# Kernel optimization log

Measured on AMD Instinct MI355X. Metric: run time of the kernel, lower is better.

The kernel has to match this reference:

```python
import jax, jax.numpy as jnp
import numpy as np

DIM_Q = 512
DIM_K = 512
DIM_V = 512
NUM_HEADS = 8
LN_EPS = 1e-5


def setup_inputs() -> dict:
    key = jax.random.key(0)
    ks = jax.random.split(key, 12)
    s_q = 1.0 / np.sqrt(DIM_Q)
    s_k = 1.0 / np.sqrt(DIM_K)
    s_v = 1.0 / np.sqrt(DIM_V)
    return {
        "Q": jax.random.normal(ks[0], (8, 1024, DIM_Q), dtype=jnp.float32),
        "K": jax.random.normal(ks[1], (8, 1024, DIM_K), dtype=jnp.float32),
        "Wq": jax.random.uniform(ks[2], (DIM_Q, DIM_V), jnp.float32, -s_q, s_q),
        "bq": jax.random.uniform(ks[3], (DIM_V,), jnp.float32, -s_q, s_q),
        "Wk": jax.random.uniform(ks[4], (DIM_K, DIM_V), jnp.float32, -s_k, s_k),
        "bk": jax.random.uniform(ks[5], (DIM_V,), jnp.float32, -s_k, s_k),
        "Wv": jax.random.uniform(ks[6], (DIM_K, DIM_V), jnp.float32, -s_k, s_k),
        "bv": jax.random.uniform(ks[7], (DIM_V,), jnp.float32, -s_k, s_k),
        "Wo": jax.random.uniform(ks[8], (DIM_V, DIM_V), jnp.float32, -s_v, s_v),
        "bo": jax.random.uniform(ks[9], (DIM_V,), jnp.float32, -s_v, s_v),
        "g0": jnp.ones((DIM_V,), jnp.float32),
        "b0": jnp.zeros((DIM_V,), jnp.float32),
        "g1": jnp.ones((DIM_V,), jnp.float32),
        "b1": jnp.zeros((DIM_V,), jnp.float32),
    }


def _layer_norm(x, gamma, beta):
    mu = jnp.mean(x, axis=-1, keepdims=True)
    var = jnp.var(x, axis=-1, keepdims=True)
    return (x - mu) * jax.lax.rsqrt(var + LN_EPS) * gamma + beta


def reference(Q, K, Wq, bq, Wk, bk, Wv, bv, Wo, bo, g0, b0, g1, b1):
    B, Nq, _ = Q.shape
    Nk = K.shape[1]
    H = NUM_HEADS
    d = DIM_V // H  # head dim

    Qp = Q @ Wq + bq                      # [B, Nq, dim_V]
    Kp = K @ Wk + bk                      # [B, Nk, dim_V]
    Vp = K @ Wv + bv                      # [B, Nk, dim_V]

    Qh = Qp.reshape(B, Nq, H, d)
    Kh = Kp.reshape(B, Nk, H, d)
    Vh = Vp.reshape(B, Nk, H, d)

    scores = jnp.einsum("bqhd,bkhd->bhqk", Qh, Kh) / jnp.sqrt(jnp.float32(d))
    A = jax.nn.softmax(scores, axis=-1)   # [B, H, Nq, Nk]
    Oh = jnp.einsum("bhqk,bkhd->bqhd", A, Vh) + Qh  # residual with projected Q
    O = Oh.reshape(B, Nq, DIM_V)

    O = _layer_norm(O, g0, b0)
    O = O + jax.nn.relu(O @ Wo + bo)
    O = _layer_norm(O, g1, b1)
    return O
```

## Files before the change

kernel.cpp:

```cpp
#include <hip/hip_runtime.h>
#include <math.h>

#define DV 512
#define HD 64
#define NHEADS 8
#define SEQ 1024
#define NBATCH 8
#define MROWS (NBATCH * SEQ)

typedef __bf16 bf16;
typedef __bf16 bf16x8 __attribute__((ext_vector_type(8)));
typedef __bf16 bf16x4 __attribute__((ext_vector_type(4)));
typedef float f32x4 __attribute__((ext_vector_type(4)));

__device__ inline void gload_lds16(const void* g, void* l) {
  __builtin_amdgcn_global_load_lds(
      (const __attribute__((address_space(1))) unsigned int*)g,
      (__attribute__((address_space(3))) unsigned int*)l, 16, 0, 0);
}

__global__ __launch_bounds__(256) void prep_kernel(
    const float* __restrict__ Qf, const float* __restrict__ Kf,
    bf16* __restrict__ Qb, bf16* __restrict__ Kb,
    const float* __restrict__ W0, const float* __restrict__ W1,
    const float* __restrict__ W2, const float* __restrict__ W3,
    bf16* __restrict__ T0, bf16* __restrict__ T1,
    bf16* __restrict__ T2, bf16* __restrict__ T3)
{
  const int z = blockIdx.z;
  if (z < 2) {
    const float* src = z ? Kf : Qf;
    bf16* dst = z ? Kb : Qb;
    int i = blockIdx.x * 256 + threadIdx.x;
    const float4* s = (const float4*)src;
    float4 a = s[i * 2], b = s[i * 2 + 1];
    bf16x8 o;
    o[0] = (bf16)a.x; o[1] = (bf16)a.y; o[2] = (bf16)a.z; o[3] = (bf16)a.w;
    o[4] = (bf16)b.x; o[5] = (bf16)b.y; o[6] = (bf16)b.z; o[7] = (bf16)b.w;
    *(bf16x8*)(dst + (size_t)i * 8) = o;
    return;
  }
  if (blockIdx.x >= 64) return;
  const float* W = z == 2 ? W0 : z == 3 ? W1 : z == 4 ? W2 : W3;
  bf16* WT = z == 2 ? T0 : z == 3 ? T1 : z == 4 ? T2 : T3;
  __shared__ float T[64][65];
  const int t = threadIdx.x;
  const int k0 = (blockIdx.x >> 3) * 64, n0 = (blockIdx.x & 7) * 64;
#pragma unroll
  for (int p = 0; p < 4; ++p) {
    int r = p * 16 + (t >> 4), c = (t & 15) * 4;
    float4 v = *(const float4*)&W[(size_t)(k0 + r) * DV + n0 + c];
    T[r][c] = v.x; T[r][c + 1] = v.y; T[r][c + 2] = v.z; T[r][c + 3] = v.w;
  }
  __syncthreads();
#pragma unroll
  for (int p = 0; p < 2; ++p) {
    int n = p * 32 + (t >> 3), kc = (t & 7) * 8;
    bf16x8 o;
#pragma unroll
    for (int j = 0; j < 8; ++j) o[j] = (bf16)T[kc + j][n];
    *(bf16x8*)&WT[(size_t)(n0 + n) * DV + k0 + kc] = o;
  }
}

__device__ __forceinline__ void gemm_core128_db(
    const bf16* __restrict__ A, const bf16* __restrict__ B,
    bf16* As, bf16* Bs, int m0, int n0, int Kd, f32x4 (*acc)[4])
{
  const int tid = threadIdx.x;
  const int lane = tid & 63, w = tid >> 6;
  const int wm = w >> 1, wn = w & 1;
  const int cl = lane & 15, qd = lane >> 4;

  size_t offA[4], offB[4];
  int ldsOff[4];
#pragma unroll
  for (int t = 0; t < 4; ++t) {
    int S = t * 256 + tid;
    int row = S >> 3, kq = (S & 7) ^ (row & 7);
    offA[t] = (size_t)(m0 + row) * Kd + kq * 8;
    offB[t] = (size_t)(n0 + row) * Kd + kq * 8;
    ldsOff[t] = (t * 256 + w * 64) * 8;
  }

#pragma unroll
  for (int t = 0; t < 4; ++t) {
    gload_lds16(A + offA[t], As + ldsOff[t]);
    gload_lds16(B + offB[t], Bs + ldsOff[t]);
  }

  const int nIter = Kd >> 6;
  for (int it = 0; it < nIter; ++it) {
    __syncthreads();
    const int cur = it & 1;
    if (it + 1 < nIter) {
      const size_t k0n = (size_t)(it + 1) * 64;
      const int nb = (cur ^ 1) * 8192;
#pragma unroll
      for (int t = 0; t < 4; ++t) {
        gload_lds16(A + k0n + offA[t], As + nb + ldsOff[t]);
        gload_lds16(B + k0n + offB[t], Bs + nb + ldsOff[t]);
      }
    }
    const bf16* A_ = As + cur * 8192;
    const bf16* B_ = Bs + cur * 8192;
#pragma unroll
    for (int cc = 0; cc < 2; ++cc) {
      bf16x8 af[4], bfr[4];
#pragma unroll
      for (int mi = 0; mi < 4; ++mi) {
        int row = wm * 64 + mi * 16 + cl;
        int slot = row * 8 + ((cc * 4 + qd) ^ (row & 7));
        af[mi] = *(const bf16x8*)(A_ + (size_t)slot * 8);
      }
#pragma unroll
      for (int ni = 0; ni < 4; ++ni) {
        int row = wn * 64 + ni * 16 + cl;
        int slot = row * 8 + ((cc * 4 + qd) ^ (row & 7));
        bfr[ni] = *(const bf16x8*)(B_ + (size_t)slot * 8);
      }
#pragma unroll
      for (int mi = 0; mi < 4; ++mi)
#pragma unroll
        for (int ni = 0; ni < 4; ++ni)
          acc[mi][ni] = __builtin_amdgcn_mfma_f32_16x16x32_bf16(
              af[mi], bfr[ni], acc[mi][ni], 0, 0, 0);
    }
  }
}

__global__ __launch_bounds__(256) void gemm_proj(
    const bf16* __restrict__ A0, const bf16* __restrict__ A1, const bf16* __restrict__ A2,
    const bf16* __restrict__ B0, const bf16* __restrict__ B1, const bf16* __restrict__ B2,
    const float* __restrict__ c0, const float* __restrict__ c1, const float* __restrict__ c2,
    bf16* __restrict__ O0, bf16* __restrict__ O1, bf16* __restrict__ O2)
{
  __shared__ bf16 As[2 * 128 * 64];
  __shared__ bf16 Bs[2 * 128 * 64];
  const int z = blockIdx.z;
  const bf16* A = z == 0 ? A0 : z == 1 ? A1 : A2;
  const bf16* B = z == 0 ? B0 : z == 1 ? B1 : B2;
  const float* bias = z == 0 ? c0 : z == 1 ? c1 : c2;
  bf16* C = z == 0 ? O0 : z == 1 ? O1 : O2;
  const int N = (z == 2) ? MROWS : DV;
  int bx, by;
  if (z < 2) { bx = blockIdx.x & 3;  by = blockIdx.x >> 2; }
  else       { bx = blockIdx.x & 63; by = blockIdx.x >> 6; }
  const int m0 = by * 128, n0 = bx * 128;

  f32x4 acc[4][4] = {};
  gemm_core128_db(A, B, As, Bs, m0, n0, DV, acc);

  const int lane = threadIdx.x & 63, w = threadIdx.x >> 6;
  const int wm = w >> 1, wn = w & 1;
  const int cl = lane & 15, qd = lane >> 4;
  float bcol[4] = {0.f, 0.f, 0.f, 0.f};
  if (z < 2)
#pragma unroll
    for (int ni = 0; ni < 4; ++ni) bcol[ni] = bias[n0 + wn * 64 + ni * 16 + cl];
#pragma unroll
  for (int mi = 0; mi < 4; ++mi)
#pragma unroll
    for (int r = 0; r < 4; ++r) {
      int gm = m0 + wm * 64 + mi * 16 + qd * 4 + r;
      float brow = (z == 2) ? bias[gm] : 0.f;
#pragma unroll
      for (int ni = 0; ni < 4; ++ni) {
        int gn = n0 + wn * 64 + ni * 16 + cl;
        float v = acc[mi][ni][r] + (z == 2 ? brow : bcol[ni]);
        C[(size_t)gm * N + gn] = (bf16)v;
      }
    }
}

__global__ __launch_bounds__(256) void gemm_out(
    const bf16* __restrict__ A, const bf16* __restrict__ B,
    const float* __restrict__ bias, const bf16* __restrict__ res,
    float* __restrict__ Cout)
{
  __shared__ bf16 As[2 * 128 * 64];
  __shared__ bf16 Bs[2 * 64 * 64];
  const int tid = threadIdx.x;
  const int lane = tid & 63, w = tid >> 6;
  const int wm = w >> 1, wn = w & 1;
  const int cl = lane & 15, qd = lane >> 4;
  const int m0 = blockIdx.y * 128, n0 = blockIdx.x * 64;

  size_t offA[4], offB[2];
  int ldsA[4], ldsB[2];
#pragma unroll
  for (int t = 0; t < 4; ++t) {
    int S = t * 256 + tid;
    int row = S >> 3, kq = (S & 7) ^ (row & 7);
    offA[t] = (size_t)(m0 + row) * DV + kq * 8;
    ldsA[t] = (t * 256 + w * 64) * 8;
  }
#pragma unroll
  for (int t = 0; t < 2; ++t) {
    int S = t * 256 + tid;
    int row = S >> 3, kq = (S & 7) ^ (row & 7);
    offB[t] = (size_t)(n0 + row) * DV + kq * 8;
    ldsB[t] = (t * 256 + w * 64) * 8;
  }

#pragma unroll
  for (int t = 0; t < 4; ++t) gload_lds16(A + offA[t], As + ldsA[t]);
#pragma unroll
  for (int t = 0; t < 2; ++t) gload_lds16(B + offB[t], Bs + ldsB[t]);

  f32x4 acc[4][2] = {};
  for (int it = 0; it < DV / 64; ++it) {
    __syncthreads();
    const int cur = it & 1;
    if (it + 1 < DV / 64) {
      const size_t k0n = (size_t)(it + 1) * 64;
#pragma unroll
      for (int t = 0; t < 4; ++t)
        gload_lds16(A + k0n + offA[t], As + (cur ^ 1) * 8192 + ldsA[t]);
#pragma unroll
      for (int t = 0; t < 2; ++t)
        gload_lds16(B + k0n + offB[t], Bs + (cur ^ 1) * 4096 + ldsB[t]);
    }
    const bf16* A_ = As + cur * 8192;
    const bf16* B_ = Bs + cur * 4096;
#pragma unroll
    for (int cc = 0; cc < 2; ++cc) {
      bf16x8 af[4], bfr[2];
#pragma unroll
      for (int mi = 0; mi < 4; ++mi) {
        int row = wm * 64 + mi * 16 + cl;
        int slot = row * 8 + ((cc * 4 + qd) ^ (row & 7));
        af[mi] = *(const bf16x8*)(A_ + (size_t)slot * 8);
      }
#pragma unroll
      for (int ni = 0; ni < 2; ++ni) {
        int row = wn * 32 + ni * 16 + cl;
        int slot = row * 8 + ((cc * 4 + qd) ^ (row & 7));
        bfr[ni] = *(const bf16x8*)(B_ + (size_t)slot * 8);
      }
#pragma unroll
      for (int mi = 0; mi < 4; ++mi)
#pragma unroll
        for (int ni = 0; ni < 2; ++ni)
          acc[mi][ni] = __builtin_amdgcn_mfma_f32_16x16x32_bf16(
              af[mi], bfr[ni], acc[mi][ni], 0, 0, 0);
    }
  }

  float bcol[2] = { bias[n0 + wn * 32 + cl], bias[n0 + wn * 32 + 16 + cl] };
#pragma unroll
  for (int mi = 0; mi < 4; ++mi)
#pragma unroll
    for (int r = 0; r < 4; ++r) {
      int gm = m0 + wm * 64 + mi * 16 + qd * 4 + r;
#pragma unroll
      for (int ni = 0; ni < 2; ++ni) {
        int gn = n0 + wn * 32 + ni * 16 + cl;
        size_t off = (size_t)gm * DV + gn;
        float v = acc[mi][ni][r] + bcol[ni];
        Cout[off] = (float)res[off] + fmaxf(v, 0.f);
      }
    }
}

__global__ __launch_bounds__(256) void attn_mfma(
    const bf16* __restrict__ Qp, const bf16* __restrict__ Kp,
    const bf16* __restrict__ VpT, bf16* __restrict__ Orb)
{
  __shared__ bf16 Ks[2][64 * 64];
  __shared__ bf16 Vs[2][64 * 64];
  __shared__ bf16 Ps[4][32 * 72];

  const int tid = threadIdx.x, lane = tid & 63, w = tid >> 6;
  const int cl = lane & 15, qd = lane >> 4;
  const int bh = blockIdx.y, b = bh >> 3, h = bh & 7;
  const int q0w = blockIdx.x * 128 + w * 32;

  const float SCL = 0.18033688011112042f;
  bf16x8 qa[2][2];
#pragma unroll
  for (int qt = 0; qt < 2; ++qt)
#pragma unroll
    for (int ch = 0; ch < 2; ++ch) {
      bf16x8 v = *(const bf16x8*)(Qp + ((size_t)b * SEQ + q0w + qt * 16 + cl) * DV
                                  + h * HD + ch * 32 + qd * 8);
#pragma unroll
      for (int j = 0; j < 8; ++j) v[j] = (bf16)((float)v[j] * SCL);
      qa[qt][ch] = v;
    }

  f32x4 o[4][2] = {};
  float lrun[2] = {0.f, 0.f};

  const bf16* Kbase = Kp + (size_t)b * SEQ * DV + h * HD;
  const bf16* Vbase = VpT + (size_t)h * HD * MROWS + (size_t)b * SEQ;
  bf16* Pw = &Ps[w][0];

  const int Sa = tid, Sb = 256 + tid;
  const int kRowA = Sa >> 3, kDgA = (Sa & 7) ^ (kRowA & 7);
  const int kRowB = Sb >> 3, kDgB = (Sb & 7) ^ (kRowB & 7);
  const size_t kOffA = (size_t)kRowA * DV + kDgA * 8;
  const size_t kOffB = (size_t)kRowB * DV + kDgB * 8;
  const size_t vOffA = (size_t)kRowA * MROWS + kDgA * 8;
  const size_t vOffB = (size_t)kRowB * MROWS + kDgB * 8;

  gload_lds16(Kbase + kOffA, &Ks[0][(size_t)(w * 64) * 8]);
  gload_lds16(Kbase + kOffB, &Ks[0][(size_t)(256 + w * 64) * 8]);
  gload_lds16(Vbase + vOffA, &Vs[0][(size_t)(w * 64) * 8]);
  gload_lds16(Vbase + vOffB, &Vs[0][(size_t)(256 + w * 64) * 8]);

  for (int it = 0; it < SEQ / 64; ++it) {
    __syncthreads();
    const int cur = it & 1;
    if (it + 1 < SEQ / 64) {
      const size_t kt = (size_t)(it + 1) * 64;
      gload_lds16(Kbase + kt * DV + kOffA, &Ks[cur ^ 1][(size_t)(w * 64) * 8]);
      gload_lds16(Kbase + kt * DV + kOffB, &Ks[cur ^ 1][(size_t)(256 + w * 64) * 8]);
      gload_lds16(Vbase + kt + vOffA, &Vs[cur ^ 1][(size_t)(w * 64) * 8]);
      gload_lds16(Vbase + kt + vOffB, &Vs[cur ^ 1][(size_t)(256 + w * 64) * 8]);
    }
    const bf16* K_ = &Ks[cur][0];
    const bf16* V_ = &Vs[cur][0];

    f32x4 sc[4][2] = {};
#pragma unroll
    for (int ch = 0; ch < 2; ++ch) {
      bf16x8 kf[4];
#pragma unroll
      for (int kt4 = 0; kt4 < 4; ++kt4) {
        int key = kt4 * 16 + cl;
        int slot = key * 8 + ((ch * 4 + qd) ^ (key & 7));
        kf[kt4] = *(const bf16x8*)(K_ + (size_t)slot * 8);
      }
#pragma unroll
      for (int kt4 = 0; kt4 < 4; ++kt4)
#pragma unroll
        for (int qt = 0; qt < 2; ++qt)
          sc[kt4][qt] = __builtin_amdgcn_mfma_f32_16x16x32_bf16(
              kf[kt4], qa[qt][ch], sc[kt4][qt], 0, 0, 0);
    }

#pragma unroll
    for (int qt = 0; qt < 2; ++qt) {
      float sum = 0.f;
#pragma unroll
      for (int kt4 = 0; kt4 < 4; ++kt4) {
        float p0 = __builtin_amdgcn_exp2f(sc[kt4][qt][0]);
        float p1 = __builtin_amdgcn_exp2f(sc[kt4][qt][1]);
        float p2 = __builtin_amdgcn_exp2f(sc[kt4][qt][2]);
        float p3 = __builtin_amdgcn_exp2f(sc[kt4][qt][3]);
        sum += (p0 + p1) + (p2 + p3);
        bf16x4 pk;
        pk[0] = (bf16)p0; pk[1] = (bf16)p1; pk[2] = (bf16)p2; pk[3] = (bf16)p3;
        *(bf16x4*)(Pw + (size_t)(qt * 16 + cl) * 72 + kt4 * 16 + qd * 4) = pk;
      }
      sum += __shfl_xor(sum, 16);
      sum += __shfl_xor(sum, 32);
      lrun[qt] += sum;
    }

#pragma unroll
    for (int kc = 0; kc < 2; ++kc) {
      bf16x8 pb[2];
#pragma unroll
      for (int qt = 0; qt < 2; ++qt)
        pb[qt] = *(const bf16x8*)(Pw + (size_t)(qt * 16 + cl) * 72 + kc * 32 + qd * 8);
#pragma unroll
      for (int dt = 0; dt < 4; ++dt) {
        int d = dt * 16 + cl;
        int slot = d * 8 + ((kc * 4 + qd) ^ (d & 7));
        bf16x8 vf = *(const bf16x8*)(V_ + (size_t)slot * 8);
#pragma unroll
        for (int qt = 0; qt < 2; ++qt)
          o[dt][qt] = __builtin_amdgcn_mfma_f32_16x16x32_bf16(
              vf, pb[qt], o[dt][qt], 0, 0, 0);
      }
    }
  }

#pragma unroll
  for (int qt = 0; qt < 2; ++qt) {
    float inv = 1.f / lrun[qt];
    size_t rowoff = ((size_t)b * SEQ + q0w + qt * 16 + cl) * DV + h * HD;
#pragma unroll
    for (int dt = 0; dt < 4; ++dt) {
      bf16x4 rv = *(const bf16x4*)(Qp + rowoff + dt * 16 + qd * 4);
      bf16x4 st;
      st[0] = (bf16)(o[dt][qt][0] * inv + (float)rv[0]);
      st[1] = (bf16)(o[dt][qt][1] * inv + (float)rv[1]);
      st[2] = (bf16)(o[dt][qt][2] * inv + (float)rv[2]);
      st[3] = (bf16)(o[dt][qt][3] * inv + (float)rv[3]);
      *(bf16x4*)(Orb + rowoff + dt * 16 + qd * 4) = st;
    }
  }
}

__global__ __launch_bounds__(256) void ln_bf16(
    const bf16* __restrict__ X, const float* __restrict__ g,
    const float* __restrict__ be, bf16* __restrict__ Y)
{
  const int row = blockIdx.x * 4 + (threadIdx.x >> 6);
  const int l = threadIdx.x & 63;
  bf16x8 xv = *(const bf16x8*)(X + (size_t)row * DV + l * 8);
  float x[8];
#pragma unroll
  for (int j = 0; j < 8; ++j) x[j] = (float)xv[j];
  float s = 0.f, s2 = 0.f;
#pragma unroll
  for (int j = 0; j < 8; ++j) { s += x[j]; s2 += x[j] * x[j]; }
#pragma unroll
  for (int off = 1; off < 64; off <<= 1) {
    s += __shfl_xor(s, off);
    s2 += __shfl_xor(s2, off);
  }
  float mu = s * (1.f / DV);
  float var = s2 * (1.f / DV) - mu * mu;
  float inv = rsqrtf(var + 1e-5f);
  float4 g1 = ((const float4*)(g + l * 8))[0], g2 = ((const float4*)(g + l * 8))[1];
  float4 b1 = ((const float4*)(be + l * 8))[0], b2 = ((const float4*)(be + l * 8))[1];
  bf16x8 ov;
  ov[0] = (bf16)((x[0] - mu) * inv * g1.x + b1.x);
  ov[1] = (bf16)((x[1] - mu) * inv * g1.y + b1.y);
  ov[2] = (bf16)((x[2] - mu) * inv * g1.z + b1.z);
  ov[3] = (bf16)((x[3] - mu) * inv * g1.w + b1.w);
  ov[4] = (bf16)((x[4] - mu) * inv * g2.x + b2.x);
  ov[5] = (bf16)((x[5] - mu) * inv * g2.y + b2.y);
  ov[6] = (bf16)((x[6] - mu) * inv * g2.z + b2.z);
  ov[7] = (bf16)((x[7] - mu) * inv * g2.w + b2.w);
  *(bf16x8*)(Y + (size_t)row * DV + l * 8) = ov;
}

__global__ __launch_bounds__(256) void ln_inplace(
    float* __restrict__ X, const float* __restrict__ g, const float* __restrict__ be)
{
  const int row = blockIdx.x * 4 + (threadIdx.x >> 6);
  const int l = threadIdx.x & 63;
  float* x = X + (size_t)row * DV + l * 8;
  float4 a = ((const float4*)x)[0], c = ((const float4*)x)[1];
  float s  = (a.x + a.y) + (a.z + a.w) + (c.x + c.y) + (c.z + c.w);
  float s2 = a.x*a.x + a.y*a.y + a.z*a.z + a.w*a.w + c.x*c.x + c.y*c.y + c.z*c.z + c.w*c.w;
#pragma unroll
  for (int off = 1; off < 64; off <<= 1) {
    s += __shfl_xor(s, off);
    s2 += __shfl_xor(s2, off);
  }
  float mu = s * (1.f / DV);
  float var = s2 * (1.f / DV) - mu * mu;
  float inv = rsqrtf(var + 1e-5f);
  float4 g1 = ((const float4*)(g + l * 8))[0], g2 = ((const float4*)(g + l * 8))[1];
  float4 b1 = ((const float4*)(be + l * 8))[0], b2 = ((const float4*)(be + l * 8))[1];
  a.x = (a.x - mu) * inv * g1.x + b1.x;
  a.y = (a.y - mu) * inv * g1.y + b1.y;
  a.z = (a.z - mu) * inv * g1.z + b1.z;
  a.w = (a.w - mu) * inv * g1.w + b1.w;
  c.x = (c.x - mu) * inv * g2.x + b2.x;
  c.y = (c.y - mu) * inv * g2.y + b2.y;
  c.z = (c.z - mu) * inv * g2.z + b2.z;
  c.w = (c.w - mu) * inv * g2.w + b2.w;
  ((float4*)x)[0] = a;
  ((float4*)x)[1] = c;
}

extern "C" void kernel_launch(void* const* d_in, const int* in_sizes, int n_in,
                              void* d_out, int out_size, void* d_ws, size_t ws_size,
                              hipStream_t stream)
{
  const float* Q  = (const float*)d_in[0];
  const float* Kf = (const float*)d_in[1];
  const float* Wq = (const float*)d_in[2];
  const float* bq = (const float*)d_in[3];
  const float* Wk = (const float*)d_in[4];
  const float* bk = (const float*)d_in[5];
  const float* Wv = (const float*)d_in[6];
  const float* bv = (const float*)d_in[7];
  const float* Wo = (const float*)d_in[8];
  const float* bo = (const float*)d_in[9];
  const float* g0 = (const float*)d_in[10];
  const float* b0 = (const float*)d_in[11];
  const float* g1 = (const float*)d_in[12];
  const float* b1 = (const float*)d_in[13];
  float* out = (float*)d_out;

  const size_t MB = 1ull << 20;
  char* W = (char*)d_ws;
  bf16* Qb  = (bf16*)(W + 0);
  bf16* Kb  = (bf16*)(W + 8 * MB);
  bf16* Qp  = (bf16*)(W + 16 * MB);
  bf16* Kp  = (bf16*)(W + 24 * MB);
  bf16* VpT = (bf16*)(W + 32 * MB);
  bf16* WqT = (bf16*)(W + 40 * MB);
  bf16* WkT = (bf16*)(W + 40 * MB + 512 * 1024);
  bf16* WvT = (bf16*)(W + 41 * MB);
  bf16* WoT = (bf16*)(W + 41 * MB + 512 * 1024);
  bf16* Xb  = (bf16*)(W + 42 * MB);
  bf16* Orb = (bf16*)(W + 0);

  dim3 blk(256);
  prep_kernel<<<dim3(2048, 1, 6), blk, 0, stream>>>(
      Q, Kf, Qb, Kb, Wq, Wk, Wv, Wo, WqT, WkT, WvT, WoT);
  gemm_proj<<<dim3(256, 1, 3), blk, 0, stream>>>(
      Qb, Kb, WvT, WqT, WkT, Kb, bq, bk, bv, Qp, Kp, VpT);
  attn_mfma<<<dim3(SEQ / 128, NBATCH * NHEADS), blk, 0, stream>>>(Qp, Kp, VpT, Orb);
  ln_bf16<<<dim3(MROWS / 4), blk, 0, stream>>>(Orb, g0, b0, Xb);
  gemm_out<<<dim3(DV / 64, MROWS / 128), blk, 0, stream>>>(Xb, WoT, bo, Xb, out);
  ln_inplace<<<dim3(MROWS / 4), blk, 0, stream>>>(out, g1, b1);
}
```

Measured before the change: 190.8 us.

## Fuse fp32-to-bf16 cast into projection GEMM and fuse LN0+out-GEMM+LN1

The projection GEMM now reads the fp32 Q and K directly, converting to bf16 in registers before storing to LDS. This removes the separate cast pass and its bf16 round-trip through memory. The tail is merged into one kernel: it layer-normalises a 32-row tile into LDS, multiplies it by WoT streamed in 32-wide k-chunks, then applies bias, ReLU and residual and runs the second layer norm in registers with a cross-wave reduction. This cuts three launches and several full-tensor round-trips, at the cost of heavy register use (64 floats plus a y array), fewer blocks, and a single-buffered WoT load with two barriers per iteration.

```diff
diff --git a/kernel.cpp b/kernel.cpp
--- a/kernel.cpp
+++ b/kernel.cpp
@@ -19,30 +19,15 @@
       (__attribute__((address_space(3))) unsigned int*)l, 16, 0, 0);
 }
 
-__global__ __launch_bounds__(256) void prep_kernel(
-    const float* __restrict__ Qf, const float* __restrict__ Kf,
-    bf16* __restrict__ Qb, bf16* __restrict__ Kb,
+__global__ __launch_bounds__(256) void prep_w(
     const float* __restrict__ W0, const float* __restrict__ W1,
     const float* __restrict__ W2, const float* __restrict__ W3,
     bf16* __restrict__ T0, bf16* __restrict__ T1,
     bf16* __restrict__ T2, bf16* __restrict__ T3)
 {
   const int z = blockIdx.z;
-  if (z < 2) {
-    const float* src = z ? Kf : Qf;
-    bf16* dst = z ? Kb : Qb;
-    int i = blockIdx.x * 256 + threadIdx.x;
-    const float4* s = (const float4*)src;
-    float4 a = s[i * 2], b = s[i * 2 + 1];
-    bf16x8 o;
-    o[0] = (bf16)a.x; o[1] = (bf16)a.y; o[2] = (bf16)a.z; o[3] = (bf16)a.w;
-    o[4] = (bf16)b.x; o[5] = (bf16)b.y; o[6] = (bf16)b.z; o[7] = (bf16)b.w;
-    *(bf16x8*)(dst + (size_t)i * 8) = o;
-    return;
-  }
-  if (blockIdx.x >= 64) return;
-  const float* W = z == 2 ? W0 : z == 3 ? W1 : z == 4 ? W2 : W3;
-  bf16* WT = z == 2 ? T0 : z == 3 ? T1 : z == 4 ? T2 : T3;
+  const float* W = z == 0 ? W0 : z == 1 ? W1 : z == 2 ? W2 : W3;
+  bf16* WT = z == 0 ? T0 : z == 1 ? T1 : z == 2 ? T2 : T3;
   __shared__ float T[64][65];
   const int t = threadIdx.x;
   const int k0 = (blockIdx.x >> 3) * 64, n0 = (blockIdx.x & 7) * 64;
@@ -63,9 +48,10 @@
   }
 }
 
-__device__ __forceinline__ void gemm_core128_db(
-    const bf16* __restrict__ A, const bf16* __restrict__ B,
-    bf16* As, bf16* Bs, int m0, int n0, int Kd, f32x4 (*acc)[4])
+template<bool AF, bool BF>
+__device__ __forceinline__ void proj_core(
+    const float* Af, const bf16* Ab, const float* Bf, const bf16* Bb,
+    bf16* As, bf16* Bs, int m0, int n0, f32x4 (*acc)[4])
 {
   const int tid = threadIdx.x;
   const int lane = tid & 63, w = tid >> 6;
@@ -73,33 +59,58 @@
   const int cl = lane & 15, qd = lane >> 4;
 
   size_t offA[4], offB[4];
-  int ldsOff[4];
+  int uOff[4], sOff[4];
 #pragma unroll
   for (int t = 0; t < 4; ++t) {
     int S = t * 256 + tid;
     int row = S >> 3, kq = (S & 7) ^ (row & 7);
-    offA[t] = (size_t)(m0 + row) * Kd + kq * 8;
-    offB[t] = (size_t)(n0 + row) * Kd + kq * 8;
-    ldsOff[t] = (t * 256 + w * 64) * 8;
-  }
+    offA[t] = (size_t)(m0 + row) * DV + kq * 8;
+    offB[t] = (size_t)(n0 + row) * DV + kq * 8;
+    uOff[t] = (t * 256 + w * 64) * 8;
+    sOff[t] = S * 8;
+  }
+
+  float4 ra0[4], ra1[4], rb0[4], rb1[4];
 
 #pragma unroll
   for (int t = 0; t < 4; ++t) {
-    gload_lds16(A + offA[t], As + ldsOff[t]);
-    gload_lds16(B + offB[t], Bs + ldsOff[t]);
-  }
-
-  const int nIter = Kd >> 6;
-  for (int it = 0; it < nIter; ++it) {
+    if (AF) {
+      ra0[t] = *(const float4*)(Af + offA[t]);
+      ra1[t] = *(const float4*)(Af + offA[t] + 4);
+      bf16x8 o;
+      o[0]=(bf16)ra0[t].x; o[1]=(bf16)ra0[t].y; o[2]=(bf16)ra0[t].z; o[3]=(bf16)ra0[t].w;
+      o[4]=(bf16)ra1[t].x; o[5]=(bf16)ra1[t].y; o[6]=(bf16)ra1[t].z; o[7]=(bf16)ra1[t].w;
+      *(bf16x8*)(As + sOff[t]) = o;
+    } else {
+      gload_lds16(Ab + offA[t], As + uOff[t]);
+    }
+    if (BF) {
+      rb0[t] = *(const float4*)(Bf + offB[t]);
+      rb1[t] = *(const float4*)(Bf + offB[t] + 4);
+      bf16x8 o;
+      o[0]=(bf16)rb0[t].x; o[1]=(bf16)rb0[t].y; o[2]=(bf16)rb0[t].z; o[3]=(bf16)rb0[t].w;
+      o[4]=(bf16)rb1[t].x; o[5]=(bf16)rb1[t].y; o[6]=(bf16)rb1[t].z; o[7]=(bf16)rb1[t].w;
+      *(bf16x8*)(Bs + sOff[t]) = o;
+    } else {
+      gload_lds16(Bb + offB[t], Bs + uOff[t]);
+    }
+  }
+
+  for (int it = 0; it < 8; ++it) {
     __syncthreads();
     const int cur = it & 1;
-    if (it + 1 < nIter) {
-      const size_t k0n = (size_t)(it + 1) * 64;
-      const int nb = (cur ^ 1) * 8192;
+    const int nb = (cur ^ 1) * 8192;
+    const bool has = (it + 1 < 8);
+    const size_t k0n = (size_t)(it + 1) * 64;
+    if (has) {
 #pragma unroll
       for (int t = 0; t < 4; ++t) {
-        gload_lds16(A + k0n + offA[t], As + nb + ldsOff[t]);
-        gload_lds16(B + k0n + offB[t], Bs + nb + ldsOff[t]);
+        if (AF) { ra0[t] = *(const float4*)(Af + k0n + offA[t]);
+                  ra1[t] = *(const float4*)(Af + k0n + offA[t] + 4); }
+        else    gload_lds16(Ab + k0n + offA[t], As + nb + uOff[t]);
+        if (BF) { rb0[t] = *(const float4*)(Bf + k0n + offB[t]);
+                  rb1[t] = *(const float4*)(Bf + k0n + offB[t] + 4); }
+        else    gload_lds16(Bb + k0n + offB[t], Bs + nb + uOff[t]);
       }
     }
     const bf16* A_ = As + cur * 8192;
@@ -126,30 +137,48 @@
           acc[mi][ni] = __builtin_amdgcn_mfma_f32_16x16x32_bf16(
               af[mi], bfr[ni], acc[mi][ni], 0, 0, 0);
     }
+    if (has) {
+#pragma unroll
+      for (int t = 0; t < 4; ++t) {
+        if (AF) {
+          bf16x8 o;
+          o[0]=(bf16)ra0[t].x; o[1]=(bf16)ra0[t].y; o[2]=(bf16)ra0[t].z; o[3]=(bf16)ra0[t].w;
+          o[4]=(bf16)ra1[t].x; o[5]=(bf16)ra1[t].y; o[6]=(bf16)ra1[t].z; o[7]=(bf16)ra1[t].w;
+          *(bf16x8*)(As + nb + sOff[t]) = o;
+        }
+        if (BF) {
+          bf16x8 o;
+          o[0]=(bf16)rb0[t].x; o[1]=(bf16)rb0[t].y; o[2]=(bf16)rb0[t].z; o[3]=(bf16)rb0[t].w;
+          o[4]=(bf16)rb1[t].x; o[5]=(bf16)rb1[t].y; o[6]=(bf16)rb1[t].z; o[7]=(bf16)rb1[t].w;
+          *(bf16x8*)(Bs + nb + sOff[t]) = o;
+        }
+      }
+    }
   }
 }
 
 __global__ __launch_bounds__(256) void gemm_proj(
-    const bf16* __restrict__ A0, const bf16* __restrict__ A1, const bf16* __restrict__ A2,
-    const bf16* __restrict__ B0, const bf16* __restrict__ B1, const bf16* __restrict__ B2,
-    const float* __restrict__ c0, const float* __restrict__ c1, const float* __restrict__ c2,
-    bf16* __restrict__ O0, bf16* __restrict__ O1, bf16* __restrict__ O2)
+    const float* __restrict__ Qf, const float* __restrict__ Kf,
+    const bf16* __restrict__ WqT, const bf16* __restrict__ WkT,
+    const bf16* __restrict__ WvT,
+    const float* __restrict__ bq, const float* __restrict__ bk,
+    const float* __restrict__ bv,
+    bf16* __restrict__ Qp, bf16* __restrict__ Kp, bf16* __restrict__ VpT)
 {
-  __shared__ bf16 As[2 * 128 * 64];
-  __shared__ bf16 Bs[2 * 128 * 64];
+  __shared__ bf16 As[2 * 8192];
+  __shared__ bf16 Bs[2 * 8192];
   const int z = blockIdx.z;
-  const bf16* A = z == 0 ? A0 : z == 1 ? A1 : A2;
-  const bf16* B = z == 0 ? B0 : z == 1 ? B1 : B2;
-  const float* bias = z == 0 ? c0 : z == 1 ? c1 : c2;
-  bf16* C = z == 0 ? O0 : z == 1 ? O1 : O2;
-  const int N = (z == 2) ? MROWS : DV;
-  int bx, by;
-  if (z < 2) { bx = blockIdx.x & 3;  by = blockIdx.x >> 2; }
-  else       { bx = blockIdx.x & 63; by = blockIdx.x >> 6; }
+  int bx, by, N;
+  if (z < 2) { bx = blockIdx.x & 3;  by = blockIdx.x >> 2; N = DV; }
+  else       { bx = blockIdx.x & 63; by = blockIdx.x >> 6; N = MROWS; }
   const int m0 = by * 128, n0 = bx * 128;
 
   f32x4 acc[4][4] = {};
-  gemm_core128_db(A, B, As, Bs, m0, n0, DV, acc);
+  const float* bias;
+  bf16* C;
+  if (z == 0) { proj_core<true,  false>(Qf, nullptr, nullptr, WqT, As, Bs, m0, n0, acc); bias = bq; C = Qp; }
+  else if (z == 1) { proj_core<true,  false>(Kf, nullptr, nullptr, WkT, As, Bs, m0, n0, acc); bias = bk; C = Kp; }
+  else { proj_core<false, true>(nullptr, WvT, Kf, nullptr, As, Bs, m0, n0, acc); bias = bv; C = VpT; }
 
   const int lane = threadIdx.x & 63, w = threadIdx.x >> 6;
   const int wm = w >> 1, wn = w & 1;
@@ -169,96 +198,6 @@
         int gn = n0 + wn * 64 + ni * 16 + cl;
         float v = acc[mi][ni][r] + (z == 2 ? brow : bcol[ni]);
         C[(size_t)gm * N + gn] = (bf16)v;
-      }
-    }
-}
-
-__global__ __launch_bounds__(256) void gemm_out(
-    const bf16* __restrict__ A, const bf16* __restrict__ B,
-    const float* __restrict__ bias, const bf16* __restrict__ res,
-    float* __restrict__ Cout)
-{
-  __shared__ bf16 As[2 * 128 * 64];
-  __shared__ bf16 Bs[2 * 64 * 64];
-  const int tid = threadIdx.x;
-  const int lane = tid & 63, w = tid >> 6;
-  const int wm = w >> 1, wn = w & 1;
-  const int cl = lane & 15, qd = lane >> 4;
-  const int m0 = blockIdx.y * 128, n0 = blockIdx.x * 64;
-
-  size_t offA[4], offB[2];
-  int ldsA[4], ldsB[2];
-#pragma unroll
-  for (int t = 0; t < 4; ++t) {
-    int S = t * 256 + tid;
-    int row = S >> 3, kq = (S & 7) ^ (row & 7);
-    offA[t] = (size_t)(m0 + row) * DV + kq * 8;
-    ldsA[t] = (t * 256 + w * 64) * 8;
-  }
-#pragma unroll
-  for (int t = 0; t < 2; ++t) {
-    int S = t * 256 + tid;
-    int row = S >> 3, kq = (S & 7) ^ (row & 7);
-    offB[t] = (size_t)(n0 + row) * DV + kq * 8;
-    ldsB[t] = (t * 256 + w * 64) * 8;
-  }
-
-#pragma unroll
-  for (int t = 0; t < 4; ++t) gload_lds16(A + offA[t], As + ldsA[t]);
-#pragma unroll
-  for (int t = 0; t < 2; ++t) gload_lds16(B + offB[t], Bs + ldsB[t]);
-
-  f32x4 acc[4][2] = {};
-  for (int it = 0; it < DV / 64; ++it) {
-    __syncthreads();
-    const int cur = it & 1;
-    if (it + 1 < DV / 64) {
-      const size_t k0n = (size_t)(it + 1) * 64;
-#pragma unroll
-      for (int t = 0; t < 4; ++t)
-        gload_lds16(A + k0n + offA[t], As + (cur ^ 1) * 8192 + ldsA[t]);
-#pragma unroll
-      for (int t = 0; t < 2; ++t)
-        gload_lds16(B + k0n + offB[t], Bs + (cur ^ 1) * 4096 + ldsB[t]);
-    }
-    const bf16* A_ = As + cur * 8192;
-    const bf16* B_ = Bs + cur * 4096;
-#pragma unroll
-    for (int cc = 0; cc < 2; ++cc) {
-      bf16x8 af[4], bfr[2];
-#pragma unroll
-      for (int mi = 0; mi < 4; ++mi) {
-        int row = wm * 64 + mi * 16 + cl;
-        int slot = row * 8 + ((cc * 4 + qd) ^ (row & 7));
-        af[mi] = *(const bf16x8*)(A_ + (size_t)slot * 8);
-      }
-#pragma unroll
-      for (int ni = 0; ni < 2; ++ni) {
-        int row = wn * 32 + ni * 16 + cl;
-        int slot = row * 8 + ((cc * 4 + qd) ^ (row & 7));
-        bfr[ni] = *(const bf16x8*)(B_ + (size_t)slot * 8);
-      }
-#pragma unroll
-      for (int mi = 0; mi < 4; ++mi)
-#pragma unroll
-        for (int ni = 0; ni < 2; ++ni)
-          acc[mi][ni] = __builtin_amdgcn_mfma_f32_16x16x32_bf16(
-              af[mi], bfr[ni], acc[mi][ni], 0, 0, 0);
-    }
-  }
-
-  float bcol[2] = { bias[n0 + wn * 32 + cl], bias[n0 + wn * 32 + 16 + cl] };
-#pragma unroll
-  for (int mi = 0; mi < 4; ++mi)
-#pragma unroll
-    for (int r = 0; r < 4; ++r) {
-      int gm = m0 + wm * 64 + mi * 16 + qd * 4 + r;
-#pragma unroll
-      for (int ni = 0; ni < 2; ++ni) {
-        int gn = n0 + wn * 32 + ni * 16 + cl;
-        size_t off = (size_t)gm * DV + gn;
-        float v = acc[mi][ni][r] + bcol[ni];
-        Cout[off] = (float)res[off] + fmaxf(v, 0.f);
       }
     }
 }
@@ -395,70 +334,156 @@
   }
 }
 
-__global__ __launch_bounds__(256) void ln_bf16(
-    const bf16* __restrict__ X, const float* __restrict__ g,
-    const float* __restrict__ be, bf16* __restrict__ Y)
+__global__ __launch_bounds__(256) void gemm_fused(
+    const bf16* __restrict__ Orb, const bf16* __restrict__ WoT,
+    const float* __restrict__ bo,
+    const float* __restrict__ g0, const float* __restrict__ b0,
+    const float* __restrict__ g1, const float* __restrict__ b1,
+    float* __restrict__ out)
 {
-  const int row = blockIdx.x * 4 + (threadIdx.x >> 6);
-  const int l = threadIdx.x & 63;
-  bf16x8 xv = *(const bf16x8*)(X + (size_t)row * DV + l * 8);
-  float x[8];
-#pragma unroll
-  for (int j = 0; j < 8; ++j) x[j] = (float)xv[j];
-  float s = 0.f, s2 = 0.f;
-#pragma unroll
-  for (int j = 0; j < 8; ++j) { s += x[j]; s2 += x[j] * x[j]; }
-#pragma unroll
-  for (int off = 1; off < 64; off <<= 1) {
-    s += __shfl_xor(s, off);
-    s2 += __shfl_xor(s2, off);
-  }
-  float mu = s * (1.f / DV);
-  float var = s2 * (1.f / DV) - mu * mu;
-  float inv = rsqrtf(var + 1e-5f);
-  float4 g1 = ((const float4*)(g + l * 8))[0], g2 = ((const float4*)(g + l * 8))[1];
-  float4 b1 = ((const float4*)(be + l * 8))[0], b2 = ((const float4*)(be + l * 8))[1];
-  bf16x8 ov;
-  ov[0] = (bf16)((x[0] - mu) * inv * g1.x + b1.x);
-  ov[1] = (bf16)((x[1] - mu) * inv * g1.y + b1.y);
-  ov[2] = (bf16)((x[2] - mu) * inv * g1.z + b1.z);
-  ov[3] = (bf16)((x[3] - mu) * inv * g1.w + b1.w);
-  ov[4] = (bf16)((x[4] - mu) * inv * g2.x + b2.x);
-  ov[5] = (bf16)((x[5] - mu) * inv * g2.y + b2.y);
-  ov[6] = (bf16)((x[6] - mu) * inv * g2.z + b2.z);
-  ov[7] = (bf16)((x[7] - mu) * inv * g2.w + b2.w);
-  *(bf16x8*)(Y + (size_t)row * DV + l * 8) = ov;
-}
-
-__global__ __launch_bounds__(256) void ln_inplace(
-    float* __restrict__ X, const float* __restrict__ g, const float* __restrict__ be)
-{
-  const int row = blockIdx.x * 4 + (threadIdx.x >> 6);
-  const int l = threadIdx.x & 63;
-  float* x = X + (size_t)row * DV + l * 8;
-  float4 a = ((const float4*)x)[0], c = ((const float4*)x)[1];
-  float s  = (a.x + a.y) + (a.z + a.w) + (c.x + c.y) + (c.z + c.w);
-  float s2 = a.x*a.x + a.y*a.y + a.z*a.z + a.w*a.w + c.x*c.x + c.y*c.y + c.z*c.z + c.w*c.w;
-#pragma unroll
-  for (int off = 1; off < 64; off <<= 1) {
-    s += __shfl_xor(s, off);
-    s2 += __shfl_xor(s2, off);
-  }
-  float mu = s * (1.f / DV);
-  float var = s2 * (1.f / DV) - mu * mu;
-  float inv = rsqrtf(var + 1e-5f);
-  float4 g1 = ((const float4*)(g + l * 8))[0], g2 = ((const float4*)(g + l * 8))[1];
-  float4 b1 = ((const float4*)(be + l * 8))[0], b2 = ((const float4*)(be + l * 8))[1];
-  a.x = (a.x - mu) * inv * g1.x + b1.x;
-  a.y = (a.y - mu) * inv * g1.y + b1.y;
-  a.z = (a.z - mu) * inv * g1.z + b1.z;
-  a.w = (a.w - mu) * inv * g1.w + b1.w;
-  c.x = (c.x - mu) * inv * g2.x + b2.x;
-  c.y = (c.y - mu) * inv * g2.y + b2.y;
-  c.z = (c.z - mu) * inv * g2.z + b2.z;
-  c.w = (c.w - mu) * inv * g2.w + b2.w;
-  ((float4*)x)[0] = a;
-  ((float4*)x)[1] = c;
+  __shared__ bf16 Bsm[32 * 512];
+  __shared__ bf16 As[2048 * 8];
+  const int tid = threadIdx.x, lane = tid & 63, w = tid >> 6;
+  const int cl = lane & 15, qd = lane >> 4;
+  const int m0 = blockIdx.x * 32;
+
+  {
+    const int q = tid >> 3, c0 = (tid & 7) * 64;
+    const bf16* src = Orb + (size_t)(m0 + q) * DV + c0;
+    float x[64];
+    float s = 0.f, s2 = 0.f;
+#pragma unroll
+    for (int j = 0; j < 8; ++j) {
+      bf16x8 xv = *(const bf16x8*)(src + j * 8);
+#pragma unroll
+      for (int e = 0; e < 8; ++e) {
+        float f = (float)xv[e];
+        x[j * 8 + e] = f; s += f; s2 += f * f;
+      }
+    }
+    s  += __shfl_xor(s, 1);  s  += __shfl_xor(s, 2);  s  += __shfl_xor(s, 4);
+    s2 += __shfl_xor(s2, 1); s2 += __shfl_xor(s2, 2); s2 += __shfl_xor(s2, 4);
+    float mu = s * (1.f / DV);
+    float inv = rsqrtf(s2 * (1.f / DV) - mu * mu + 1e-5f);
+#pragma unroll
+    for (int j = 0; j < 8; ++j) {
+      float4 ga = *(const float4*)(g0 + c0 + j * 8);
+      float4 gb = *(const float4*)(g0 + c0 + j * 8 + 4);
+      float4 ba = *(const float4*)(b0 + c0 + j * 8);
+      float4 bb = *(const float4*)(b0 + c0 + j * 8 + 4);
+      bf16x8 o;
+      o[0] = (bf16)((x[j*8+0] - mu) * inv * ga.x + ba.x);
+      o[1] = (bf16)((x[j*8+1] - mu) * inv * ga.y + ba.y);
+      o[2] = (bf16)((x[j*8+2] - mu) * inv * ga.z + ba.z);
+      o[3] = (bf16)((x[j*8+3] - mu) * inv * ga.w + ba.w);
+      o[4] = (bf16)((x[j*8+4] - mu) * inv * gb.x + bb.x);
+      o[5] = (bf16)((x[j*8+5] - mu) * inv * gb.y + bb.y);
+      o[6] = (bf16)((x[j*8+6] - mu) * inv * gb.z + bb.z);
+      o[7] = (bf16)((x[j*8+7] - mu) * inv * gb.w + bb.w);
+      int g = (tid & 7) * 8 + j;
+      int slot = q * 64 + (g ^ (q & 7));
+      *(bf16x8*)(Bsm + (size_t)slot * 8) = o;
+    }
+  }
+  __syncthreads();
+
+  size_t offA[8];
+  int uOff[8];
+#pragma unroll
+  for (int t = 0; t < 8; ++t) {
+    int S = t * 256 + tid;
+    int frow = S >> 2, kq = (S & 3) ^ ((frow >> 1) & 3);
+    offA[t] = (size_t)frow * DV + kq * 8;
+    uOff[t] = (t * 256 + w * 64) * 8;
+  }
+
+  f32x4 acc[8][2] = {};
+  for (int it = 0; it < 16; ++it) {
+    __syncthreads();
+#pragma unroll
+    for (int t = 0; t < 8; ++t)
+      gload_lds16(WoT + (size_t)it * 32 + offA[t], As + uOff[t]);
+    __syncthreads();
+
+    bf16x8 bfr[2];
+#pragma unroll
+    for (int nt = 0; nt < 2; ++nt) {
+      int q = nt * 16 + cl;
+      int slot = q * 64 + ((it * 4 + qd) ^ (q & 7));
+      bfr[nt] = *(const bf16x8*)(Bsm + (size_t)slot * 8);
+    }
+#pragma unroll
+    for (int mt = 0; mt < 8; ++mt) {
+      int frow = (w * 8 + mt) * 16 + cl;
+      int slot = frow * 4 + (qd ^ ((frow >> 1) & 3));
+      bf16x8 af = *(const bf16x8*)(As + (size_t)slot * 8);
+#pragma unroll
+      for (int nt = 0; nt < 2; ++nt)
+        acc[mt][nt] = __builtin_amdgcn_mfma_f32_16x16x32_bf16(
+            af, bfr[nt], acc[mt][nt], 0, 0, 0);
+    }
+  }
+
+  __syncthreads();
+  float* red = (float*)As;
+  float y[8][2][4];
+  float sy[2], sy2[2];
+#pragma unroll
+  for (int nt = 0; nt < 2; ++nt) {
+    sy[nt] = 0.f; sy2[nt] = 0.f;
+    const int q = nt * 16 + cl;
+#pragma unroll
+    for (int mt = 0; mt < 8; ++mt) {
+      const int f0 = (w * 8 + mt) * 16 + qd * 4;
+      float4 bov = *(const float4*)(bo + f0);
+      int g = f0 >> 3;
+      int slot = q * 64 + (g ^ (q & 7));
+      bf16x4 rv = *(const bf16x4*)(Bsm + (size_t)slot * 8 + (qd & 1) * 4);
+      const float* bp = (const float*)&bov;
+#pragma unroll
+      for (int r = 0; r < 4; ++r) {
+        float v = fmaxf(acc[mt][nt][r] + bp[r], 0.f) + (float)rv[r];
+        y[mt][nt][r] = v;
+        sy[nt] += v; sy2[nt] += v * v;
+      }
+    }
+    sy[nt]  += __shfl_xor(sy[nt], 16);  sy[nt]  += __shfl_xor(sy[nt], 32);
+    sy2[nt] += __shfl_xor(sy2[nt], 16); sy2[nt] += __shfl_xor(sy2[nt], 32);
+  }
+  if (qd == 0) {
+#pragma unroll
+    for (int nt = 0; nt < 2; ++nt) {
+      int q = nt * 16 + cl;
+      red[(q * 4 + w) * 2 + 0] = sy[nt];
+      red[(q * 4 + w) * 2 + 1] = sy2[nt];
+    }
+  }
+  __syncthreads();
+#pragma unroll
+  for (int nt = 0; nt < 2; ++nt) {
+    const int q = nt * 16 + cl;
+    float s = 0.f, s2 = 0.f;
+#pragma unroll
+    for (int ww = 0; ww < 4; ++ww) {
+      s  += red[(q * 4 + ww) * 2 + 0];
+      s2 += red[(q * 4 + ww) * 2 + 1];
+    }
+    float mu1 = s * (1.f / DV);
+    float inv1 = rsqrtf(s2 * (1.f / DV) - mu1 * mu1 + 1e-5f);
+    size_t rowoff = (size_t)(m0 + q) * DV;
+#pragma unroll
+    for (int mt = 0; mt < 8; ++mt) {
+      const int f0 = (w * 8 + mt) * 16 + qd * 4;
+      float4 gv = *(const float4*)(g1 + f0);
+      float4 bv = *(const float4*)(b1 + f0);
+      float4 ov;
+      ov.x = (y[mt][nt][0] - mu1) * inv1 * gv.x + bv.x;
+      ov.y = (y[mt][nt][1] - mu1) * inv1 * gv.y + bv.y;
+      ov.z = (y[mt][nt][2] - mu1) * inv1 * gv.z + bv.z;
+      ov.w = (y[mt][nt][3] - mu1) * inv1 * gv.w + bv.w;
+      *(float4*)(out + rowoff + f0) = ov;
+    }
+  }
 }
 
 extern "C" void kernel_launch(void* const* d_in, const int* in_sizes, int n_in,
@@ -483,25 +508,20 @@
 
   const size_t MB = 1ull << 20;
   char* W = (char*)d_ws;
-  bf16* Qb  = (bf16*)(W + 0);
-  bf16* Kb  = (bf16*)(W + 8 * MB);
-  bf16* Qp  = (bf16*)(W + 16 * MB);
-  bf16* Kp  = (bf16*)(W + 24 * MB);
-  bf16* VpT = (bf16*)(W + 32 * MB);
-  bf16* WqT = (bf16*)(W + 40 * MB);
-  bf16* WkT = (bf16*)(W + 40 * MB + 512 * 1024);
-  bf16* WvT = (bf16*)(W + 41 * MB);
-  bf16* WoT = (bf16*)(W + 41 * MB + 512 * 1024);
-  bf16* Xb  = (bf16*)(W + 42 * MB);
   bf16* Orb = (bf16*)(W + 0);
+  bf16* Qp  = (bf16*)(W + 8 * MB);
+  bf16* Kp  = (bf16*)(W + 16 * MB);
+  bf16* VpT = (bf16*)(W + 24 * MB);
+  bf16* WqT = (bf16*)(W + 32 * MB);
+  bf16* WkT = (bf16*)(W + 32 * MB + 512 * 1024);
+  bf16* WvT = (bf16*)(W + 33 * MB);
+  bf16* WoT = (bf16*)(W + 33 * MB + 512 * 1024);
 
   dim3 blk(256);
-  prep_kernel<<<dim3(2048, 1, 6), blk, 0, stream>>>(
-      Q, Kf, Qb, Kb, Wq, Wk, Wv, Wo, WqT, WkT, WvT, WoT);
+  prep_w<<<dim3(64, 1, 4), blk, 0, stream>>>(Wq, Wk, Wv, Wo, WqT, WkT, WvT, WoT);
   gemm_proj<<<dim3(256, 1, 3), blk, 0, stream>>>(
-      Qb, Kb, WvT, WqT, WkT, Kb, bq, bk, bv, Qp, Kp, VpT);
+      Q, Kf, WqT, WkT, WvT, bq, bk, bv, Qp, Kp, VpT);
   attn_mfma<<<dim3(SEQ / 128, NBATCH * NHEADS), blk, 0, stream>>>(Qp, Kp, VpT, Orb);
-  ln_bf16<<<dim3(MROWS / 4), blk, 0, stream>>>(Orb, g0, b0, Xb);
-  gemm_out<<<dim3(DV / 64, MROWS / 128), blk, 0, stream>>>(Xb, WoT, bo, Xb, out);
-  ln_inplace<<<dim3(MROWS / 4), blk, 0, stream>>>(out, g1, b1);
-}
+  gemm_fused<<<dim3(MROWS / 32), blk, 0, stream>>>(
+      Orb, WoT, bo, g0, b0, g1, b1, out);
+}
```

After: 197.3 us. 3.4% more time.
